# Kernel tuning notes

Hardware: AMD Instinct MI355X
Metric: run time of the kernel (lower is better)

## Reference

```python
import jax, jax.numpy as jnp
import numpy as np

C_TOTAL = 201      # n_classes + 1 (background)
N_CLASSES = 200
K = 5              # n_prototypes
DIM = 768
GAMMA = 0.999
TEMPERATURE = 0.2
THRESH = 0.8       # assignment_threshold


def l2norm(x, axis=-1, eps=1e-12):
    return x / jnp.maximum(jnp.linalg.norm(x, axis=axis, keepdims=True), eps)


def setup_inputs() -> dict:
    key = jax.random.key(0)
    k0, k1, k2, k3, k4 = jax.random.split(key, 5)
    B, H, W = 32, 32, 32
    N = H * W
    patch_tokens = jax.random.normal(k0, (B, N, DIM), jnp.float32)
    raw_patch_tokens = jax.random.normal(k1, (B, N, DIM), jnp.float32)
    # trunc_normal_(std=0.02) init of the prototype buffer
    prototypes = jax.random.truncated_normal(k2, -2.0, 2.0, (C_TOTAL, K, DIM), jnp.float32) * 0.02
    sa_weights = jnp.ones((N_CLASSES, K), jnp.float32)  # constant init -> uniform softmax, same as 0.5
    labels = jax.random.randint(k3, (32,), 0, N_CLASSES)
    sam_masks = jax.random.randint(k4, (B, H, W), 0, 2, dtype=jnp.int32)
    return {
        'patch_tokens': patch_tokens,
        'raw_patch_tokens': raw_patch_tokens,
        'prototypes': prototypes,
        'sa_weights': sa_weights,
        'labels': labels,
        'sam_masks': sam_masks,
    }


def reference(patch_tokens, raw_patch_tokens, prototypes, sa_weights, labels, sam_masks):
    B, N, D = patch_tokens.shape
    H = W = int(np.sqrt(N))

    # --- prototype matching ---
    pt = l2norm(patch_tokens)
    proto_n = l2norm(prototypes)
    # [B, N, C, K] cosine logits
    logits = jnp.einsum('bnd,ckd->bnck', pt, proto_n)
    image_prototype_logits = logits.max(axis=1)                    # [B, C, K]
    saw = jax.nn.softmax(sa_weights, axis=-1) * K                  # ScoreAggregation
    class_logits = (image_prototype_logits[:, :-1, :] * saw).sum(-1) / TEMPERATURE  # [B, n_classes]

    # --- pseudo patch labels (sam_masks already at (H, W) -> nearest interp is identity) ---
    pm = sam_masks.astype(jnp.float32)                             # [B, H, W]
    pseudo = jnp.where(pm == 1.0, labels[:, None, None], N_CLASSES)  # [B, H, W] int

    # --- online clustering (vectorized over the per-class python loop) ---
    raw = l2norm(raw_patch_tokens).reshape(B * N, D)               # detached in original
    lab_flat = pseudo.reshape(-1)                                  # [BN]
    L = logits.reshape(B * N, C_TOTAL, K)
    # gather each token's logits for its own (pseudo) class: L[n, lab_flat[n], :]
    Lc = jnp.take_along_axis(L, lab_flat[:, None, None], axis=1)[:, 0, :]  # [BN, K]
    A = jax.nn.softmax(Lc, axis=-1)
    max_vals = A.max(axis=-1)
    indices = A.argmax(axis=-1)
    # threshold then L1-renormalize (zero rows stay zero, matching F.normalize eps)
    A = jnp.where(max_vals[:, None] < THRESH, 0.0, A)
    A = A / jnp.maximum(A.sum(axis=-1, keepdims=True), 1e-12)
    # per-class soft-kmeans centroid accumulation: P_c_new = A_c^T @ I_c
    wx = A[:, :, None] * raw[:, None, :]                           # [BN, K, D]
    P_c_new = jax.ops.segment_sum(wx, lab_flat, num_segments=C_TOTAL)  # [C, K, D]
    counts = jax.ops.segment_sum(jnp.ones_like(lab_flat), lab_flat, num_segments=C_TOTAL)
    present = (counts > 0)[:, None, None]
    # momentum EMA update, only for classes present in the batch
    P_new = jnp.where(present, GAMMA * prototypes + (1.0 - GAMMA) * P_c_new, prototypes)

    part_assignment_maps = (indices + lab_flat * K).reshape(B, H * W)

    return (class_logits, image_prototype_logits, logits, part_assignment_maps, P_new, pseudo)
```

## Files before the change

### kernel.cpp

```cpp
#include <hip/hip_runtime.h>
#include <math.h>

#define Bv   32
#define Nv   1024
#define Dv   768
#define Cv   201
#define Kv   5
#define CKv  1005
#define BNv  32768
#define NCLS 200

#define OFF_CL     0
#define OFF_IPL    6400
#define OFF_LOG    38560
#define OFF_PART   32970400
#define OFF_PNEW   33003168
#define OFF_PSEUDO 33775008

typedef short bf16x8 __attribute__((ext_vector_type(8)));
typedef float f32x4  __attribute__((ext_vector_type(4)));
typedef float f32x4u __attribute__((ext_vector_type(4), aligned(4)));
typedef __attribute__((address_space(1))) const unsigned int g_u32;
typedef __attribute__((address_space(3))) unsigned int l_u32;

__device__ inline unsigned short f2bf(float f) {
  unsigned u = __float_as_uint(f);
  u += 0x7fffu + ((u >> 16) & 1u);
  return (unsigned short)(u >> 16);
}
__device__ inline float bf2f(unsigned short h) {
  return __uint_as_float(((unsigned)h) << 16);
}
__device__ inline unsigned fenc(float f) {
  unsigned u = __float_as_uint(f);
  return u ^ (((unsigned)((int)u >> 31)) | 0x80000000u);
}
__device__ inline float fdec(unsigned u) {
  unsigned bits = (u & 0x80000000u) ? (u ^ 0x80000000u) : ~u;
  return __uint_as_float(bits);
}

__global__ __launch_bounds__(256) void prep_kernel(
    const float* __restrict__ pt, const float* __restrict__ raw,
    const float* __restrict__ proto,
    unsigned short* __restrict__ Ah, unsigned short* __restrict__ Bhl,
    float* __restrict__ inv_raw, int* __restrict__ zbuf, int zn, int ZB) {
  if ((int)blockIdx.x < ZB) {
    int i = blockIdx.x * 256 + threadIdx.x;
    if (i < zn) zbuf[i] = 0;
    return;
  }
  int row = (blockIdx.x - ZB) * 4 + (threadIdx.x >> 6);
  int l   = threadIdx.x & 63;

  if (row < BNv) {
    const float* src = pt + (size_t)row * Dv;
    unsigned short* dst = Ah + (size_t)row * Dv;
    float4 v[3];
    float s = 0.f;
#pragma unroll
    for (int i = 0; i < 3; ++i) {
      v[i] = reinterpret_cast<const float4*>(src)[i * 64 + l];
      s += v[i].x * v[i].x + v[i].y * v[i].y + v[i].z * v[i].z + v[i].w * v[i].w;
    }
#pragma unroll
    for (int off = 32; off > 0; off >>= 1) s += __shfl_xor(s, off);
    float inv = 1.0f / fmaxf(sqrtf(s), 1e-12f);
#pragma unroll
    for (int i = 0; i < 3; ++i) {
      float a[4] = {v[i].x * inv, v[i].y * inv, v[i].z * inv, v[i].w * inv};
      *reinterpret_cast<ushort4*>(dst + i * 256 + 4 * l) =
          make_ushort4(f2bf(a[0]), f2bf(a[1]), f2bf(a[2]), f2bf(a[3]));
    }
    return;
  }
  if (row < BNv + 1024) {
    int rp = row - BNv;
    unsigned short* dst = Bhl + (size_t)rp * 1536;
    if (rp >= CKv) {
      ushort4 z = make_ushort4(0, 0, 0, 0);
#pragma unroll
      for (int i = 0; i < 3; ++i) {
        int db = 8 * i + (l >> 3);
        int base = db * 64 + 4 * (l & 7);
        *reinterpret_cast<ushort4*>(dst + base)      = z;
        *reinterpret_cast<ushort4*>(dst + base + 32) = z;
      }
      return;
    }
    const float* src = proto + (size_t)rp * Dv;
    float4 v[3];
    float s = 0.f;
#pragma unroll
    for (int i = 0; i < 3; ++i) {
      v[i] = reinterpret_cast<const float4*>(src)[i * 64 + l];
      s += v[i].x * v[i].x + v[i].y * v[i].y + v[i].z * v[i].z + v[i].w * v[i].w;
    }
#pragma unroll
    for (int off = 32; off > 0; off >>= 1) s += __shfl_xor(s, off);
    float inv = 1.0f / fmaxf(sqrtf(s), 1e-12f);
#pragma unroll
    for (int i = 0; i < 3; ++i) {
      float a[4] = {v[i].x * inv, v[i].y * inv, v[i].z * inv, v[i].w * inv};
      unsigned short hh[4], ll[4];
#pragma unroll
      for (int t = 0; t < 4; ++t) {
        hh[t] = f2bf(a[t]);
        ll[t] = f2bf(a[t] - bf2f(hh[t]));
      }
      int db = 8 * i + (l >> 3);
      int base = db * 64 + 4 * (l & 7);
      *reinterpret_cast<ushort4*>(dst + base)      = make_ushort4(hh[0], hh[1], hh[2], hh[3]);
      *reinterpret_cast<ushort4*>(dst + base + 32) = make_ushort4(ll[0], ll[1], ll[2], ll[3]);
    }
    return;
  }
  if (row < 2 * BNv + 1024) {
    int rr = row - BNv - 1024;
    const float* src = raw + (size_t)rr * Dv;
    float s = 0.f;
#pragma unroll
    for (int i = 0; i < 3; ++i) {
      float4 v = reinterpret_cast<const float4*>(src)[i * 64 + l];
      s += v.x * v.x + v.y * v.y + v.z * v.z + v.w * v.w;
    }
#pragma unroll
    for (int off = 32; off > 0; off >>= 1) s += __shfl_xor(s, off);
    if (l == 0) inv_raw[rr] = 1.0f / fmaxf(sqrtf(s), 1e-12f);
  }
}

#define BM 256
#define BN 128
__global__ __launch_bounds__(512) void gemm_mfma_kernel(
    const unsigned short* __restrict__ Ah, const unsigned short* __restrict__ Bhl,
    float* __restrict__ Co, unsigned int* __restrict__ iplU) {
  __shared__ __align__(16) unsigned char smem[65536];
#define LA(b) ((unsigned short (*)[32])(smem + (b) * 16384))
#define LB(b) ((unsigned short (*)[64])(smem + 32768 + (b) * 16384))
  const int tid  = threadIdx.x;
  const int wid  = tid >> 6;
  const int lane = tid & 63;
  const int wm = wid >> 1, wn = wid & 1;
  const int m0 = blockIdx.x * BM, n0 = blockIdx.y * BN;
  const int fr = lane & 15;
  const int q  = lane >> 4;

  f32x4 acc[4][4];
#pragma unroll
  for (int i = 0; i < 4; ++i)
#pragma unroll
    for (int j = 0; j < 4; ++j)
#pragma unroll
      for (int r = 0; r < 4; ++r) acc[i][j][r] = 0.f;

  const int raA = wid * 16 + (lane >> 2);
  const int saA = (lane & 3) ^ ((raA >> 1) & 3);
  const unsigned short* srcA0 = Ah + (size_t)(m0 + raA) * Dv + saA * 8;
  const unsigned short* srcA1 = Ah + (size_t)(m0 + 128 + raA) * Dv + saA * 8;
  const int rbB = wid * 8 + (lane >> 3);
  const int sbB = (lane & 7) ^ (rbB & 7);
  const unsigned short* srcB0 = Bhl + (size_t)(n0 + rbB) * 1536 + sbB * 8;
  const unsigned short* srcB1 = Bhl + (size_t)(n0 + 64 + rbB) * 1536 + sbB * 8;

#define STG_A0(buf, t) __builtin_amdgcn_global_load_lds((g_u32*)(srcA0 + (t) * 32), \
    (l_u32*)&LA(buf)[wid * 16][0], 16, 0, 0)
#define STG_A1(buf, t) __builtin_amdgcn_global_load_lds((g_u32*)(srcA1 + (t) * 32), \
    (l_u32*)&LA(buf)[128 + wid * 16][0], 16, 0, 0)
#define STG_B0(buf, t) __builtin_amdgcn_global_load_lds((g_u32*)(srcB0 + (t) * 64), \
    (l_u32*)&LB(buf)[wid * 8][0], 16, 0, 0)
#define STG_B1(buf, t) __builtin_amdgcn_global_load_lds((g_u32*)(srcB1 + (t) * 64), \
    (l_u32*)&LB(buf)[64 + wid * 8][0], 16, 0, 0)

  const int slotA = (q ^ ((fr >> 1) & 3)) * 8;
  const int shB   = (q ^ (fr & 7)) * 8;
  const int slB   = ((q + 4) ^ (fr & 7)) * 8;

  STG_A0(0, 0); STG_A1(0, 0); STG_B0(0, 0); STG_B1(0, 0);

#pragma unroll 2
  for (int t = 0; t < 24; ++t) {
    const int cur = t & 1;
    if (t < 23) {
      STG_A0(cur ^ 1, t + 1); STG_A1(cur ^ 1, t + 1);
      STG_B0(cur ^ 1, t + 1); STG_B1(cur ^ 1, t + 1);
      asm volatile("s_waitcnt vmcnt(4)" ::: "memory");
    } else {
      asm volatile("s_waitcnt vmcnt(0)" ::: "memory");
    }
    __builtin_amdgcn_s_barrier();
    __builtin_amdgcn_sched_barrier(0);

    bf16x8 a[4];
#pragma unroll
    for (int j = 0; j < 4; ++j) {
      if (j == 0) {
#pragma unroll
        for (int i = 0; i < 4; ++i)
          a[i] = *reinterpret_cast<const bf16x8*>(&LA(cur)[wm * 64 + i * 16 + fr][slotA]);
      }
      const unsigned short* pb = &LB(cur)[wn * 64 + j * 16 + fr][0];
      bf16x8 bh = *reinterpret_cast<const bf16x8*>(pb + shB);
      bf16x8 bl = *reinterpret_cast<const bf16x8*>(pb + slB);
      asm volatile("s_waitcnt lgkmcnt(0)" ::: "memory");
      __builtin_amdgcn_sched_barrier(0);
      __builtin_amdgcn_s_setprio(1);
#pragma unroll
      for (int i = 0; i < 4; ++i) {
        acc[i][j] = __builtin_amdgcn_mfma_f32_16x16x32_bf16(a[i], bh, acc[i][j], 0, 0, 0);
        acc[i][j] = __builtin_amdgcn_mfma_f32_16x16x32_bf16(a[i], bl, acc[i][j], 0, 0, 0);
      }
      __builtin_amdgcn_s_setprio(0);
      __builtin_amdgcn_sched_barrier(0);
      __builtin_amdgcn_s_barrier();
      __builtin_amdgcn_sched_barrier(0);
    }
  }
#undef STG_A0
#undef STG_A1
#undef STG_B0
#undef STG_B1

  const int b_img = m0 >> 10;
#pragma unroll
  for (int j = 0; j < 4; ++j) {
    int n = n0 + wn * 64 + j * 16 + fr;
    bool ok = (n < CKv);
    float cmax = -INFINITY;
#pragma unroll
    for (int i = 0; i < 4; ++i)
#pragma unroll
      for (int r = 0; r < 4; ++r) cmax = fmaxf(cmax, acc[i][j][r]);
    cmax = fmaxf(cmax, __shfl_xor(cmax, 16));
    cmax = fmaxf(cmax, __shfl_xor(cmax, 32));
    if (lane < 16 && ok)
      atomicMax(&iplU[(size_t)b_img * 1024 + n], fenc(cmax));
  }

  float (*ebuf)[132] = (float (*)[132])smem;
  const int r2 = lane >> 5;
  const int cl = (lane & 31) * 4;
#pragma unroll
  for (int p = 0; p < 4; ++p) {
    __syncthreads();
    if (wm == p) {
#pragma unroll
      for (int i = 0; i < 4; ++i)
#pragma unroll
        for (int j = 0; j < 4; ++j)
#pragma unroll
          for (int r = 0; r < 4; ++r)
            ebuf[i * 16 + q * 4 + r][wn * 64 + j * 16 + fr] = acc[i][j][r];
    }
    __syncthreads();
#pragma unroll
    for (int rr = 0; rr < 8; rr += 2) {
      int row = wid * 8 + rr + r2;
      f32x4 v = *reinterpret_cast<const f32x4*>(&ebuf[row][cl]);
      int gc = n0 + cl;
      size_t base = (size_t)(m0 + p * 64 + row) * CKv + gc;
      if (gc + 3 < CKv) {
        *reinterpret_cast<f32x4u*>(&Co[base]) = v;
      } else {
#pragma unroll
        for (int e = 0; e < 4; ++e)
          if (gc + e < CKv) Co[base + e] = v[e];
      }
    }
  }
#undef LA
#undef LB
}

__global__ __launch_bounds__(256) void assign_ipl_kernel(
    const float* __restrict__ logits, const int* __restrict__ labels,
    const int* __restrict__ sam, float* __restrict__ out,
    float* __restrict__ A_buf, int* __restrict__ tok_lab,
    int* __restrict__ present,
    const unsigned int* __restrict__ iplU, const float* __restrict__ sa_w) {
  if ((int)blockIdx.x >= BNv / 256) {
    int b = blockIdx.x - BNv / 256;
    int c = threadIdx.x;
    if (c >= Cv) return;
    float r[Kv];
#pragma unroll
    for (int k = 0; k < Kv; ++k) {
      r[k] = fdec(iplU[(size_t)b * 1024 + c * Kv + k]);
      out[OFF_IPL + (size_t)(b * Cv + c) * Kv + k] = r[k];
    }
    if (c < NCLS) {
      float w[Kv], wm = -INFINITY;
#pragma unroll
      for (int k = 0; k < Kv; ++k) { w[k] = sa_w[c * Kv + k]; wm = fmaxf(wm, w[k]); }
      float es = 0.f;
#pragma unroll
      for (int k = 0; k < Kv; ++k) { w[k] = expf(w[k] - wm); es += w[k]; }
      float cl = 0.f;
#pragma unroll
      for (int k = 0; k < Kv; ++k) cl += r[k] * (w[k] / es * (float)Kv);
      out[OFF_CL + b * NCLS + c] = cl / 0.2f;
    }
    return;
  }
  int n = blockIdx.x * 256 + threadIdx.x;
  int b = n >> 10;
  int lab = (sam[n] == 1) ? labels[b] : NCLS;
  out[OFF_PSEUDO + n] = (float)lab;
  const float* p = logits + (size_t)n * CKv + lab * Kv;
  float L[Kv];
#pragma unroll
  for (int k = 0; k < Kv; ++k) L[k] = p[k];
  float mv = L[0];
  int idx = 0;
#pragma unroll
  for (int k = 1; k < Kv; ++k)
    if (L[k] > mv) { mv = L[k]; idx = k; }
  out[OFF_PART + n] = (float)(idx + lab * Kv);
  float e[Kv], s = 0.f;
#pragma unroll
  for (int k = 0; k < Kv; ++k) { e[k] = expf(L[k] - mv); s += e[k]; }
  float inv = 1.0f / s;
  float scale = (inv < 0.8f) ? 0.f : inv;
#pragma unroll
  for (int k = 0; k < Kv; ++k) A_buf[(size_t)n * Kv + k] = e[k] * scale;
  tok_lab[n] = lab;
  present[lab] = 1;
}

__global__ __launch_bounds__(256) void accum_kernel(
    const float* __restrict__ raw, const float* __restrict__ inv_raw,
    const float* __restrict__ A_buf, const int* __restrict__ tok_lab,
    const int* __restrict__ labels, float* __restrict__ P_acc) {
  const int b = blockIdx.x;
  const int d = blockIdx.y * 256 + threadIdx.x;
  const int t0 = blockIdx.z * 128;
  __shared__ float As[128][Kv];
  __shared__ float Sc[128];
  __shared__ int   Ls[128];
  if (threadIdx.x < 128) {
    int n = b * Nv + t0 + threadIdx.x;
#pragma unroll
    for (int k = 0; k < Kv; ++k) As[threadIdx.x][k] = A_buf[(size_t)n * Kv + k];
    Ls[threadIdx.x] = tok_lab[n];
    Sc[threadIdx.x] = inv_raw[n];
  }
  __syncthreads();
  float accL[Kv] = {}, accB[Kv] = {};
#pragma unroll 4
  for (int t = 0; t < 128; ++t) {
    int n2 = b * Nv + t0 + t;
    float rv = raw[(size_t)n2 * Dv + d] * Sc[t];
    if (Ls[t] == NCLS) {
#pragma unroll
      for (int k = 0; k < Kv; ++k) accB[k] = fmaf(As[t][k], rv, accB[k]);
    } else {
#pragma unroll
      for (int k = 0; k < Kv; ++k) accL[k] = fmaf(As[t][k], rv, accL[k]);
    }
  }
  int lab = labels[b];
#pragma unroll
  for (int k = 0; k < Kv; ++k) atomicAdd(&P_acc[((size_t)lab * Kv + k) * Dv + d], accL[k]);
#pragma unroll
  for (int k = 0; k < Kv; ++k) atomicAdd(&P_acc[((size_t)NCLS * Kv + k) * Dv + d], accB[k]);
}

__global__ __launch_bounds__(256) void pnew_kernel(
    const float* __restrict__ proto, const float* __restrict__ P_acc,
    const int* __restrict__ present, float* __restrict__ out) {
  int i = blockIdx.x * 256 + threadIdx.x;
  if (i >= Cv * Kv * Dv) return;
  int c = i / (Kv * Dv);
  float p = proto[i];
  out[OFF_PNEW + i] = present[c] ? 0.999f * p + 0.001f * P_acc[i] : p;
}

extern "C" void kernel_launch(void* const* d_in, const int* in_sizes, int n_in,
                              void* d_out, int out_size, void* d_ws, size_t ws_size,
                              hipStream_t stream) {
  const float* pt     = (const float*)d_in[0];
  const float* raw    = (const float*)d_in[1];
  const float* proto  = (const float*)d_in[2];
  const float* sa_w   = (const float*)d_in[3];
  const int*   labels = (const int*)d_in[4];
  const int*   sam    = (const int*)d_in[5];
  float* out = (float*)d_out;

  float* A_buf   = (float*)d_ws;
  int*   tok_lab = (int*)(A_buf + (size_t)BNv * Kv);
  float* P_acc   = (float*)(tok_lab + BNv);
  int*   present = (int*)(P_acc + (size_t)Cv * Kv * Dv);
  unsigned int* iplU = (unsigned int*)(present + 256);
  float* inv_raw = (float*)(iplU + BNv);
  unsigned short* Ah  = (unsigned short*)(inv_raw + BNv);
  unsigned short* Bhl = Ah + (size_t)BNv * Dv;

  int nz = Cv * Kv * Dv + 256 + BNv;
  int ZB = (nz + 255) / 256;
  int prep_rows_blocks = (2 * BNv + 1024) / 4;

  prep_kernel<<<ZB + prep_rows_blocks, 256, 0, stream>>>(
      pt, raw, proto, Ah, Bhl, inv_raw, (int*)P_acc, nz, ZB);

  gemm_mfma_kernel<<<dim3(BNv / BM, 1024 / BN), 512, 0, stream>>>(
      Ah, Bhl, out + OFF_LOG, iplU);

  assign_ipl_kernel<<<BNv / 256 + Bv, 256, 0, stream>>>(
      out + OFF_LOG, labels, sam, out, A_buf, tok_lab, present, iplU, sa_w);

  accum_kernel<<<dim3(Bv, Dv / 256, Nv / 128), 256, 0, stream>>>(
      raw, inv_raw, A_buf, tok_lab, labels, P_acc);

  pnew_kernel<<<(Cv * Kv * Dv + 255) / 256, 256, 0, stream>>>(
      proto, P_acc, present, out);
}
```

Measured before the change: 214.3 us.

## Fuse assignment into accumulation and move raw-norm pass into GEMM launch

```diff
diff --git a/kernel.cpp b/kernel.cpp
--- a/kernel.cpp
+++ b/kernel.cpp
@@ -41,10 +41,9 @@
 }
 
 __global__ __launch_bounds__(256) void prep_kernel(
-    const float* __restrict__ pt, const float* __restrict__ raw,
-    const float* __restrict__ proto,
+    const float* __restrict__ pt, const float* __restrict__ proto,
     unsigned short* __restrict__ Ah, unsigned short* __restrict__ Bhl,
-    float* __restrict__ inv_raw, int* __restrict__ zbuf, int zn, int ZB) {
+    int* __restrict__ zbuf, int zn, int ZB) {
   if ((int)blockIdx.x < ZB) {
     int i = blockIdx.x * 256 + threadIdx.x;
     if (i < zn) zbuf[i] = 0;
@@ -115,25 +114,13 @@
     }
     return;
   }
-  if (row < 2 * BNv + 1024) {
-    int rr = row - BNv - 1024;
-    const float* src = raw + (size_t)rr * Dv;
-    float s = 0.f;
-#pragma unroll
-    for (int i = 0; i < 3; ++i) {
-      float4 v = reinterpret_cast<const float4*>(src)[i * 64 + l];
-      s += v.x * v.x + v.y * v.y + v.z * v.z + v.w * v.w;
-    }
-#pragma unroll
-    for (int off = 32; off > 0; off >>= 1) s += __shfl_xor(s, off);
-    if (l == 0) inv_raw[rr] = 1.0f / fmaxf(sqrtf(s), 1e-12f);
-  }
 }
 
 #define BM 256
 #define BN 128
 __global__ __launch_bounds__(512) void gemm_mfma_kernel(
     const unsigned short* __restrict__ Ah, const unsigned short* __restrict__ Bhl,
+    const float* __restrict__ raw, float* __restrict__ inv_raw,
     float* __restrict__ Co, unsigned int* __restrict__ iplU) {
   __shared__ __align__(16) unsigned char smem[65536];
 #define LA(b) ((unsigned short (*)[32])(smem + (b) * 16384))
@@ -141,8 +128,26 @@
   const int tid  = threadIdx.x;
   const int wid  = tid >> 6;
   const int lane = tid & 63;
+
+  if (blockIdx.y == 0) {
+    const int base_row = blockIdx.x * 256 + wid * 32;
+    for (int i = 0; i < 32; ++i) {
+      const float* src = raw + (size_t)(base_row + i) * Dv;
+      float s = 0.f;
+#pragma unroll
+      for (int j2 = 0; j2 < 3; ++j2) {
+        float4 v = reinterpret_cast<const float4*>(src)[j2 * 64 + lane];
+        s += v.x * v.x + v.y * v.y + v.z * v.z + v.w * v.w;
+      }
+#pragma unroll
+      for (int off = 32; off > 0; off >>= 1) s += __shfl_xor(s, off);
+      if (lane == 0) inv_raw[base_row + i] = 1.0f / fmaxf(sqrtf(s), 1e-12f);
+    }
+    return;
+  }
+
   const int wm = wid >> 1, wn = wid & 1;
-  const int m0 = blockIdx.x * BM, n0 = blockIdx.y * BN;
+  const int m0 = blockIdx.x * BM, n0 = (blockIdx.y - 1) * BN;
   const int fr = lane & 15;
   const int q  = lane >> 4;
 
@@ -272,14 +277,17 @@
 #undef LB
 }
 
-__global__ __launch_bounds__(256) void assign_ipl_kernel(
+__global__ __launch_bounds__(256) void accum_fused_kernel(
     const float* __restrict__ logits, const int* __restrict__ labels,
-    const int* __restrict__ sam, float* __restrict__ out,
-    float* __restrict__ A_buf, int* __restrict__ tok_lab,
-    int* __restrict__ present,
+    const int* __restrict__ sam, const float* __restrict__ raw,
+    const float* __restrict__ inv_raw, float* __restrict__ out,
+    float* __restrict__ P_acc, int* __restrict__ present,
     const unsigned int* __restrict__ iplU, const float* __restrict__ sa_w) {
-  if ((int)blockIdx.x >= BNv / 256) {
-    int b = blockIdx.x - BNv / 256;
+  const int b = blockIdx.x;
+  const int y = blockIdx.y;
+  const int z = blockIdx.z;
+  if (z == 8) {
+    if (y != 0) return;
     int c = threadIdx.x;
     if (c >= Cv) return;
     float r[Kv];
@@ -302,49 +310,41 @@
     }
     return;
   }
-  int n = blockIdx.x * 256 + threadIdx.x;
-  int b = n >> 10;
-  int lab = (sam[n] == 1) ? labels[b] : NCLS;
-  out[OFF_PSEUDO + n] = (float)lab;
-  const float* p = logits + (size_t)n * CKv + lab * Kv;
-  float L[Kv];
-#pragma unroll
-  for (int k = 0; k < Kv; ++k) L[k] = p[k];
-  float mv = L[0];
-  int idx = 0;
-#pragma unroll
-  for (int k = 1; k < Kv; ++k)
-    if (L[k] > mv) { mv = L[k]; idx = k; }
-  out[OFF_PART + n] = (float)(idx + lab * Kv);
-  float e[Kv], s = 0.f;
-#pragma unroll
-  for (int k = 0; k < Kv; ++k) { e[k] = expf(L[k] - mv); s += e[k]; }
-  float inv = 1.0f / s;
-  float scale = (inv < 0.8f) ? 0.f : inv;
-#pragma unroll
-  for (int k = 0; k < Kv; ++k) A_buf[(size_t)n * Kv + k] = e[k] * scale;
-  tok_lab[n] = lab;
-  present[lab] = 1;
-}
-
-__global__ __launch_bounds__(256) void accum_kernel(
-    const float* __restrict__ raw, const float* __restrict__ inv_raw,
-    const float* __restrict__ A_buf, const int* __restrict__ tok_lab,
-    const int* __restrict__ labels, float* __restrict__ P_acc) {
-  const int b = blockIdx.x;
-  const int d = blockIdx.y * 256 + threadIdx.x;
-  const int t0 = blockIdx.z * 128;
+
   __shared__ float As[128][Kv];
   __shared__ float Sc[128];
   __shared__ int   Ls[128];
+  const int t0 = z * 128;
   if (threadIdx.x < 128) {
     int n = b * Nv + t0 + threadIdx.x;
-#pragma unroll
-    for (int k = 0; k < Kv; ++k) As[threadIdx.x][k] = A_buf[(size_t)n * Kv + k];
-    Ls[threadIdx.x] = tok_lab[n];
+    int lab = (sam[n] == 1) ? labels[b] : NCLS;
+    const float* p = logits + (size_t)n * CKv + lab * Kv;
+    float L[Kv];
+#pragma unroll
+    for (int k = 0; k < Kv; ++k) L[k] = p[k];
+    float mv = L[0];
+    int idx = 0;
+#pragma unroll
+    for (int k = 1; k < Kv; ++k)
+      if (L[k] > mv) { mv = L[k]; idx = k; }
+    float e[Kv], s = 0.f;
+#pragma unroll
+    for (int k = 0; k < Kv; ++k) { e[k] = expf(L[k] - mv); s += e[k]; }
+    float inv = 1.0f / s;
+    float scale = (inv < 0.8f) ? 0.f : inv;
+#pragma unroll
+    for (int k = 0; k < Kv; ++k) As[threadIdx.x][k] = e[k] * scale;
+    Ls[threadIdx.x] = lab;
     Sc[threadIdx.x] = inv_raw[n];
+    if (y == 0) {
+      out[OFF_PSEUDO + n] = (float)lab;
+      out[OFF_PART + n] = (float)(idx + lab * Kv);
+      present[lab] = 1;
+    }
   }
   __syncthreads();
+
+  const int d = y * 256 + threadIdx.x;
   float accL[Kv] = {}, accB[Kv] = {};
 #pragma unroll 4
   for (int t = 0; t < 128; ++t) {
@@ -397,19 +397,16 @@
 
   int nz = Cv * Kv * Dv + 256 + BNv;
   int ZB = (nz + 255) / 256;
-  int prep_rows_blocks = (2 * BNv + 1024) / 4;
+  int prep_rows_blocks = (BNv + 1024) / 4;
 
   prep_kernel<<<ZB + prep_rows_blocks, 256, 0, stream>>>(
-      pt, raw, proto, Ah, Bhl, inv_raw, (int*)P_acc, nz, ZB);
-
-  gemm_mfma_kernel<<<dim3(BNv / BM, 1024 / BN), 512, 0, stream>>>(
-      Ah, Bhl, out + OFF_LOG, iplU);
-
-  assign_ipl_kernel<<<BNv / 256 + Bv, 256, 0, stream>>>(
-      out + OFF_LOG, labels, sam, out, A_buf, tok_lab, present, iplU, sa_w);
-
-  accum_kernel<<<dim3(Bv, Dv / 256, Nv / 128), 256, 0, stream>>>(
-      raw, inv_raw, A_buf, tok_lab, labels, P_acc);
+      pt, proto, Ah, Bhl, (int*)P_acc, nz, ZB);
+
+  gemm_mfma_kernel<<<dim3(BNv / BM, 1 + 1024 / BN), 512, 0, stream>>>(
+      Ah, Bhl, raw, inv_raw, out + OFF_LOG, iplU);
+
+  accum_fused_kernel<<<dim3(Bv, Dv / 256, 9), 256, 0, stream>>>(
+      out + OFF_LOG, labels, sam, raw, inv_raw, out, P_acc, present, iplU, sa_w);
 
   pnew_kernel<<<(Cv * Kv * Dv + 255) / 256, 256, 0, stream>>>(
       proto, P_acc, present, out);
```

New measurement: 220.4 us. 2.8% more time.
